# Kernel optimization log

Measured on AMD Instinct MI355X. Metric: run time of the kernel, lower is better.

## Reference

```python
import jax, jax.numpy as jnp
import numpy as np

B, T, E, H, V = 64, 32, 300, 1024, 10000


def setup_inputs() -> dict:
    key = jax.random.key(0)
    ks = jax.random.split(key, 12)
    s = lambda fan: 1.0 / np.sqrt(fan)
    return {
        "questions": jax.random.randint(ks[0], (B, T), 0, V, dtype=jnp.int64) if jax.config.jax_enable_x64 else jax.random.randint(ks[0], (B, T), 0, V, dtype=jnp.int32),
        "question_lengths": jax.random.randint(ks[1], (B,), 1, T + 1, dtype=jnp.int32),
        "embed_table": jax.random.normal(ks[2], (V, E), jnp.float32) * 0.02,
        "W_ih1": jax.random.normal(ks[3], (4 * H, E), jnp.float32) * s(H),
        "W_hh1": jax.random.normal(ks[4], (4 * H, H), jnp.float32) * s(H),
        "b_ih1": jax.random.normal(ks[5], (4 * H,), jnp.float32) * s(H),
        "b_hh1": jax.random.normal(ks[6], (4 * H,), jnp.float32) * s(H),
        "W_ih2": jax.random.normal(ks[7], (4 * H, H), jnp.float32) * s(H),
        "W_hh2": jax.random.normal(ks[8], (4 * H, H), jnp.float32) * s(H),
        "b_ih2": jax.random.normal(ks[9], (4 * H,), jnp.float32) * s(H),
        "b_hh2": jax.random.normal(ks[10], (4 * H,), jnp.float32) * s(H),
    }


def _lstm_cell(x_t, h, c, W_ih, W_hh, b_ih, b_hh):
    # PyTorch LSTMCell: gate order i, f, g, o
    gates = x_t @ W_ih.T + b_ih + h @ W_hh.T + b_hh  # [B, 4H]
    i, f, g, o = jnp.split(gates, 4, axis=-1)
    c_new = jax.nn.sigmoid(f) * c + jax.nn.sigmoid(i) * jnp.tanh(g)
    h_new = jax.nn.sigmoid(o) * jnp.tanh(c_new)
    return h_new, c_new


def reference(questions, question_lengths, embed_table,
              W_ih1, W_hh1, b_ih1, b_hh1, W_ih2, W_hh2, b_ih2, b_hh2):
    x = embed_table[questions]                      # [B, T, E]
    b, t, _ = x.shape
    h = W_hh1.shape[1]

    def step(carry, inp):
        h1, c1, h2, c2 = carry
        x_t, m = inp                                # x_t [B,E], m [B,1] bool
        h1n, c1n = _lstm_cell(x_t, h1, c1, W_ih1, W_hh1, b_ih1, b_hh1)
        h2n, c2n = _lstm_cell(h1n, h2, c2, W_ih2, W_hh2, b_ih2, b_hh2)
        # samples past their length keep their final state frozen
        h1 = jnp.where(m, h1n, h1); c1 = jnp.where(m, c1n, c1)
        h2 = jnp.where(m, h2n, h2); c2 = jnp.where(m, c2n, c2)
        return (h1, c1, h2, c2), None

    mask = jnp.arange(t)[None, :] < question_lengths[:, None]      # [B,T]
    xs = (jnp.swapaxes(x, 0, 1), jnp.swapaxes(mask, 0, 1)[..., None])
    init = tuple(jnp.zeros((b, h), x.dtype) for _ in range(4))
    (h1, c1, h2, c2), _ = jax.lax.scan(step, init, xs)

    # tile final top-layer hidden to [B, H, 28, 28]
    E_q = jnp.broadcast_to(h2[:, None, None, :], (b, 28, 28, h))
    E_q = jnp.transpose(E_q, (0, 3, 2, 1))
    return (E_q, h1[:, None, :], h2[:, None, :], c1[:, None, :], c2[:, None, :])
```

## Files before the change

### kernel.cpp

```cpp
#include <hip/hip_runtime.h>
#include <hip/hip_bf16.h>
#include <cstdint>

#define B_  64
#define T_  32
#define E_  300
#define EP  320
#define H_  1024
#define G4  4096
#define BH  65536
#define NBLK 192

typedef __attribute__((ext_vector_type(8))) short bf16x8;
typedef __attribute__((ext_vector_type(4))) float f32x4;
typedef unsigned short ushort_t;

__device__ __forceinline__ bf16x8 load_b8(const ushort_t* p) {
    union { uint4 u; bf16x8 v; } c;
    c.u = *reinterpret_cast<const uint4*>(p);
    return c.v;
}

__device__ __forceinline__ ushort_t f2bf(float x) {
    union { float f; uint32_t u; } c; c.f = x;
    uint32_t r = c.u + 0x7fffu + ((c.u >> 16) & 1u);
    return (ushort_t)(r >> 16);
}

__device__ __forceinline__ float sigm(float x) { return 1.0f / (1.0f + __expf(-x)); }

__device__ __forceinline__ void astore64(uint64_t* p, uint64_t v) {
    __hip_atomic_store(p, v, __ATOMIC_RELAXED, __HIP_MEMORY_SCOPE_AGENT);
}
__device__ __forceinline__ uint64_t packf2(float a, float b) {
    union { float f[2]; uint64_t u; } c; c.f[0] = a; c.f[1] = b; return c.u;
}

__device__ __forceinline__ void arrive(int* ctr, int t, int role, int js) {
    __hip_atomic_fetch_add(&ctr[((t * 3 + role) * 4 + (js & 3)) * 32], 1,
                           __ATOMIC_RELAXED, __HIP_MEMORY_SCOPE_AGENT);
}
__device__ __forceinline__ void waitc(int* ctr, int t, int role) {
    int sum;
    do {
        sum = 0;
        #pragma unroll
        for (int k = 0; k < 4; ++k)
            sum += __hip_atomic_load(&ctr[((t * 3 + role) * 4 + k) * 32],
                                     __ATOMIC_RELAXED, __HIP_MEMORY_SCOPE_AGENT);
        if (sum < 64) __builtin_amdgcn_s_sleep(1);
    } while (sum < 64);
}

__global__ void prep_inputs(const int* __restrict__ q, const float* __restrict__ table,
                            ushort_t* __restrict__ Xp,
                            const float* __restrict__ Wsrc, ushort_t* __restrict__ Wdst) {
    int blk = blockIdx.x;
    if (blk < 1280) {
        int i = blk * 256 + threadIdx.x;
        const int n = B_ * T_ * EP;
        for (; i < n; i += 1280 * 256) {
            int r = i / EP, c = i - r * EP;
            Xp[i] = (c < E_) ? f2bf(table[q[r] * E_ + c]) : (ushort_t)0;
        }
    } else {
        int i = (blk - 1280) * 256 + threadIdx.x;
        const int n = G4 * EP;
        for (; i < n; i += 2048 * 256) {
            int r = i / EP, c = i - r * EP;
            Wdst[i] = (c < E_) ? f2bf(Wsrc[r * E_ + c]) : (ushort_t)0;
        }
    }
}

__launch_bounds__(256)
__global__ void xgemm(const ushort_t* __restrict__ Xp, const ushort_t* __restrict__ Wp,
                      const float* __restrict__ b_ih1, const float* __restrict__ b_hh1,
                      float* __restrict__ xg) {
    int mblk = blockIdx.x, nblk = blockIdx.y;
    int wave = threadIdx.x >> 6, lane = threadIdx.x & 63;
    int lm = lane & 15, lq = lane >> 4;
    int m0 = mblk * 64 + wave * 16;
    f32x4 acc[4];
    #pragma unroll
    for (int g = 0; g < 4; ++g) {
        int n = nblk * 64 + g * 16 + lm;
        float bv = b_ih1[n] + b_hh1[n];
        acc[g] = (f32x4){bv, bv, bv, bv};
    }
    for (int k0 = 0; k0 < EP; k0 += 32) {
        bf16x8 a = load_b8(Xp + (m0 + lm) * EP + k0 + lq * 8);
        #pragma unroll
        for (int g = 0; g < 4; ++g) {
            bf16x8 b = load_b8(Wp + (nblk * 64 + g * 16 + lm) * EP + k0 + lq * 8);
            acc[g] = __builtin_amdgcn_mfma_f32_16x16x32_bf16(a, b, acc[g], 0, 0, 0);
        }
    }
    #pragma unroll
    for (int g = 0; g < 4; ++g)
        #pragma unroll
        for (int r = 0; r < 4; ++r) {
            int m = m0 + lq * 4 + r;
            int b = m >> 5, t = m & 31;
            int n = nblk * 64 + g * 16 + lm;
            xg[((size_t)t * B_ + b) * G4 + n] = acc[g][r];
        }
}


__device__ __forceinline__ void gemm_k1024(const ushort_t* __restrict__ hvec,
                                           const ushort_t (*w)[1032],
                                           int lm, int lq, int m0, f32x4 acc[4]) {
    const uint4* hr = reinterpret_cast<const uint4*>(hvec + (size_t)(m0 + lm) * H_);
    uint4 buf[32];
    #pragma unroll
    for (int grp = 0; grp < 4; ++grp)
        #pragma unroll
        for (int i = 0; i < 8; ++i)
            buf[grp * 8 + i] = hr[grp * 32 + i * 4 + lq];
    #pragma unroll
    for (int grp = 0; grp < 4; ++grp)
        #pragma unroll
        for (int i = 0; i < 8; ++i) {
            int k0 = grp * 256 + i * 32;
            union { uint4 u; bf16x8 v; } a; a.u = buf[grp * 8 + i];
            #pragma unroll
            for (int g = 0; g < 4; ++g) {
                bf16x8 bb = load_b8(&w[g * 16 + lm][k0 + lq * 8]);
                acc[g] = __builtin_amdgcn_mfma_f32_16x16x32_bf16(a.v, bb, acc[g], 0, 0, 0);
            }
        }
}

__device__ __forceinline__ void lstm_elem(const f32x4 acc[4], int r,
                                          float* c, float* h, ushort_t* hb) {
    float iv = sigm(acc[0][r]);
    float fv = sigm(acc[1][r]);
    float gv = tanhf(acc[2][r]);
    float ov = sigm(acc[3][r]);
    float cn = fv * c[r] + iv * gv;
    float hv = ov * tanhf(cn);
    c[r] = cn; h[r] = hv; hb[r] = f2bf(hv);
}

__device__ __forceinline__ void store_h_tile(ushort_t* dst, int js, const ushort_t* hst) {
    int tid = threadIdx.x;
    uint64_t v = reinterpret_cast<const uint64_t*>(hst)[tid];
    astore64(reinterpret_cast<uint64_t*>(dst + (size_t)(tid >> 2) * H_ + js * 16) + (tid & 3), v);
}

__global__ __launch_bounds__(256) void lstm_persist(
    const float* __restrict__ Whh1, const float* __restrict__ Wih2,
    const float* __restrict__ Whh2,
    const float* __restrict__ b_ih2, const float* __restrict__ b_hh2,
    const float* __restrict__ xg, const int* __restrict__ qlen,
    ushort_t* __restrict__ h1hist,
    ushort_t* __restrict__ h2hist,
    float* __restrict__ Qhist,
    float* __restrict__ h1f, float* __restrict__ c1f,
    float* __restrict__ h2f, float* __restrict__ c2f,
    int* __restrict__ ctr)
{
    __shared__ ushort_t ws[64][1032];
    __shared__ __align__(16) ushort_t hstage[64][16];

    const int blk  = blockIdx.x;
    const int role = blk >> 6;
    const int js   = blk & 63;
    const int wave = threadIdx.x >> 6, lane = threadIdx.x & 63;
    const int lm = lane & 15, lq = lane >> 4;
    const int m0 = wave * 16;

    const float* Wsrc = (role == 0) ? Whh1 : (role == 1) ? Wih2 : Whh2;
    for (int idx = threadIdx.x; idx < 64 * 256; idx += 256) {
        int r = idx >> 8, c4 = idx & 255;
        int grow = (r >> 4) * H_ + js * 16 + (r & 15);
        float4 v = reinterpret_cast<const float4*>(Wsrc + (size_t)grow * H_)[c4];
        uint2 pk;
        pk.x = (uint32_t)f2bf(v.x) | ((uint32_t)f2bf(v.y) << 16);
        pk.y = (uint32_t)f2bf(v.z) | ((uint32_t)f2bf(v.w) << 16);
        *reinterpret_cast<uint2*>(&ws[r][c4 * 4]) = pk;
    }
    __syncthreads();

    int q[4];
    #pragma unroll
    for (int r = 0; r < 4; ++r) q[r] = qlen[m0 + lq * 4 + r];

    float    c_reg[4]  = {0.f, 0.f, 0.f, 0.f};
    float    h_reg[4]  = {0.f, 0.f, 0.f, 0.f};
    ushort_t hb_reg[4] = {0, 0, 0, 0};

    if (role == 0) {
        for (int t = 0; t < T_; ++t) {
            f32x4 acc[4];
            #pragma unroll
            for (int g = 0; g < 4; ++g)
                #pragma unroll
                for (int r = 0; r < 4; ++r)
                    acc[g][r] = xg[((size_t)t * B_ + (m0 + lq * 4 + r)) * G4 + g * H_ + js * 16 + lm];
            if (t > 0) {
                if (threadIdx.x == 0) waitc(ctr, t - 1, 0);
                __syncthreads();
            }
            gemm_k1024(h1hist + (size_t)t * BH, ws, lm, lq, m0, acc);
            #pragma unroll
            for (int r = 0; r < 4; ++r) {
                if (t < q[r]) lstm_elem(acc, r, c_reg, h_reg, hb_reg);
                hstage[m0 + lq * 4 + r][lm] = hb_reg[r];
            }
            __syncthreads();
            store_h_tile(h1hist + (size_t)(t + 1) * BH, js, &hstage[0][0]);
            __syncthreads();
            if (threadIdx.x == 0) arrive(ctr, t, 0, js);
        }
        #pragma unroll
        for (int r = 0; r < 4; ++r) {
            int b = m0 + lq * 4 + r, j = js * 16 + lm;
            h1f[b * H_ + j] = h_reg[r]; c1f[b * H_ + j] = c_reg[r];
        }
    } else if (role == 1) {
        float bi[4];
        #pragma unroll
        for (int g = 0; g < 4; ++g) {
            int n = g * H_ + js * 16 + lm;
            bi[g] = b_ih2[n] + b_hh2[n];
        }
        for (int t = 0; t < T_; ++t) {
            if (threadIdx.x == 0) waitc(ctr, t, 0);
            __syncthreads();
            f32x4 acc[4];
            #pragma unroll
            for (int g = 0; g < 4; ++g) acc[g] = (f32x4){bi[g], bi[g], bi[g], bi[g]};
            gemm_k1024(h1hist + (size_t)(t + 1) * BH, ws, lm, lq, m0, acc);
            uint64_t* Qw64 = (uint64_t*)(Qhist + (size_t)t * (4 * BH));
            #pragma unroll
            for (int r = 0; r < 4; ++r) {
                int b = m0 + lq * 4 + r, j = js * 16 + lm;
                size_t base = ((size_t)b * H_ + j) * 2;
                astore64(Qw64 + base,     packf2(acc[0][r], acc[1][r]));
                astore64(Qw64 + base + 1, packf2(acc[2][r], acc[3][r]));
            }
            __syncthreads();
            if (threadIdx.x == 0) arrive(ctr, t, 1, js);
        }
    } else {
        for (int t = 0; t < T_; ++t) {
            if (threadIdx.x == 0) waitc(ctr, t, 1);
            else if (threadIdx.x == 64 && t > 0) waitc(ctr, t - 1, 2);
            __syncthreads();
            const uint4* Qr = (const uint4*)(Qhist + (size_t)t * (4 * BH));
            f32x4 acc[4];
            #pragma unroll
            for (int r = 0; r < 4; ++r) {
                uint4 p = Qr[(size_t)(m0 + lq * 4 + r) * H_ + js * 16 + lm];
                union { uint32_t u; float f; } x0, x1, x2, x3;
                x0.u = p.x; x1.u = p.y; x2.u = p.z; x3.u = p.w;
                acc[0][r] = x0.f; acc[1][r] = x1.f;
                acc[2][r] = x2.f; acc[3][r] = x3.f;
            }
            gemm_k1024(h2hist + (size_t)t * BH, ws, lm, lq, m0, acc);
            #pragma unroll
            for (int r = 0; r < 4; ++r) {
                if (t < q[r]) lstm_elem(acc, r, c_reg, h_reg, hb_reg);
                hstage[m0 + lq * 4 + r][lm] = hb_reg[r];
            }
            __syncthreads();
            store_h_tile(h2hist + (size_t)(t + 1) * BH, js, &hstage[0][0]);
            __syncthreads();
            if (t < T_ - 1 && threadIdx.x == 0) arrive(ctr, t, 2, js);
        }
        #pragma unroll
        for (int r = 0; r < 4; ++r) {
            int b = m0 + lq * 4 + r, j = js * 16 + lm;
            h2f[b * H_ + j] = h_reg[r]; c2f[b * H_ + j] = c_reg[r];
        }
    }
}

__global__ void write_out(const float* __restrict__ h1f, const float* __restrict__ h2f,
                          const float* __restrict__ c1f, const float* __restrict__ c2f,
                          float* __restrict__ out) {
    const long long EQ = (long long)B_ * H_ * 784;
    const long long n4 = (EQ + 4LL * B_ * H_) / 4;
    long long i4 = (long long)blockIdx.x * blockDim.x + threadIdx.x;
    long long stride = (long long)gridDim.x * blockDim.x;
    for (; i4 < n4; i4 += stride) {
        long long f = i4 * 4;
        float4 v;
        if (f < EQ) {
            long long bh = f / 784;
            float val = h2f[bh];
            v = make_float4(val, val, val, val);
        } else {
            long long r = f - EQ;
            int which = (int)(r >> 16);
            int j = (int)(r & 65535);
            const float* src = (which == 0) ? h1f : (which == 1) ? h2f : (which == 2) ? c1f : c2f;
            v = *reinterpret_cast<const float4*>(src + j);
        }
        reinterpret_cast<float4*>(out)[i4] = v;
    }
}

extern "C" void kernel_launch(void* const* d_in, const int* in_sizes, int n_in,
                              void* d_out, int out_size, void* d_ws, size_t ws_size,
                              hipStream_t stream) {
    const int*   questions = (const int*)d_in[0];
    const int*   qlen      = (const int*)d_in[1];
    const float* embed     = (const float*)d_in[2];
    const float* W_ih1     = (const float*)d_in[3];
    const float* W_hh1     = (const float*)d_in[4];
    const float* b_ih1     = (const float*)d_in[5];
    const float* b_hh1     = (const float*)d_in[6];
    const float* W_ih2     = (const float*)d_in[7];
    const float* W_hh2     = (const float*)d_in[8];
    const float* b_ih2     = (const float*)d_in[9];
    const float* b_hh2     = (const float*)d_in[10];
    float* out = (float*)d_out;

    char* w = (char*)d_ws;
    float*    xg     = (float*)(w + 0);
    ushort_t* Wih1p  = (ushort_t*)(w + 33554432);
    ushort_t* Xp     = (ushort_t*)(w + 36175872);
    int*      ctr    = (int*)(w + 36175872);
    ushort_t* h1hist = (ushort_t*)(w + 37486592);
    ushort_t* h2hist = (ushort_t*)(w + 41811968);
    float*    Qhist  = (float*)(w + 46137344);
    float*    h1f    = (float*)(w + 79691776);
    float*    c1f    = (float*)(w + 79953920);
    float*    h2f    = (float*)(w + 80216064);
    float*    c2f    = (float*)(w + 80478208);

    hipMemsetAsync(w + 37486592, 0, 131072, stream);
    hipMemsetAsync(w + 41811968, 0, 131072, stream);

    prep_inputs<<<3328, 256, 0, stream>>>(questions, embed, Xp, W_ih1, Wih1p);
    xgemm<<<dim3(32, 64), 256, 0, stream>>>(Xp, Wih1p, b_ih1, b_hh1, xg);

    hipMemsetAsync(w + 36175872, 0, 49152, stream);

    lstm_persist<<<NBLK, 256, 0, stream>>>(W_hh1, W_ih2, W_hh2, b_ih2, b_hh2,
                                           xg, qlen,
                                           h1hist, h2hist, Qhist,
                                           h1f, c1f, h2f, c2f, ctr);

    write_out<<<4096, 256, 0, stream>>>(h1f, h2f, c1f, c2f, out);
}
```

Baseline: 635.7 us.

## Replace atomic counter barriers with per-block step flags polled by a wave

Swaps the per-step atomic fetch-add counters, which one thread polled, for per-block monotonic step flags. A whole wave polls all 64 producer flags in parallel and checks them with a wave-wide vote. The layer-2 block now issues its Q-history load before the recurrent GEMM and adds it afterwards, so the load latency overlaps the matrix work. The flag wait also gains a bounded spin guard that silently proceeds on timeout, which could hide a deadlock as wrong results.

```diff
diff --git a/kernel.cpp b/kernel.cpp
--- a/kernel.cpp
+++ b/kernel.cpp
@@ -36,20 +36,19 @@
     union { float f[2]; uint64_t u; } c; c.f[0] = a; c.f[1] = b; return c.u;
 }
 
-__device__ __forceinline__ void arrive(int* ctr, int t, int role, int js) {
-    __hip_atomic_fetch_add(&ctr[((t * 3 + role) * 4 + (js & 3)) * 32], 1,
-                           __ATOMIC_RELAXED, __HIP_MEMORY_SCOPE_AGENT);
-}
-__device__ __forceinline__ void waitc(int* ctr, int t, int role) {
-    int sum;
-    do {
-        sum = 0;
-        #pragma unroll
-        for (int k = 0; k < 4; ++k)
-            sum += __hip_atomic_load(&ctr[((t * 3 + role) * 4 + k) * 32],
-                                     __ATOMIC_RELAXED, __HIP_MEMORY_SCOPE_AGENT);
-        if (sum < 64) __builtin_amdgcn_s_sleep(1);
-    } while (sum < 64);
+__device__ __forceinline__ void setflag(int* flags, int role, int js, int val) {
+    __hip_atomic_store(&flags[(role * 64 + js) * 16], val,
+                       __ATOMIC_RELAXED, __HIP_MEMORY_SCOPE_AGENT);
+}
+__device__ __forceinline__ void waitwave(const int* flags, int role, int target, int lane) {
+    const int* p = &flags[(role * 64 + lane) * 16];
+    int guard = 0;
+    for (;;) {
+        int v = __hip_atomic_load(p, __ATOMIC_RELAXED, __HIP_MEMORY_SCOPE_AGENT);
+        if (__all(v >= target)) return;
+        if (++guard > (1 << 22)) return;
+        __builtin_amdgcn_s_sleep(1);
+    }
 }
 
 __global__ void prep_inputs(const int* __restrict__ q, const float* __restrict__ table,
@@ -159,7 +158,7 @@
     float* __restrict__ Qhist,
     float* __restrict__ h1f, float* __restrict__ c1f,
     float* __restrict__ h2f, float* __restrict__ c2f,
-    int* __restrict__ ctr)
+    int* __restrict__ flags)
 {
     __shared__ ushort_t ws[64][1032];
     __shared__ __align__(16) ushort_t hstage[64][16];
@@ -200,7 +199,7 @@
                 for (int r = 0; r < 4; ++r)
                     acc[g][r] = xg[((size_t)t * B_ + (m0 + lq * 4 + r)) * G4 + g * H_ + js * 16 + lm];
             if (t > 0) {
-                if (threadIdx.x == 0) waitc(ctr, t - 1, 0);
+                if (wave == 0) waitwave(flags, 0, t, lane);
                 __syncthreads();
             }
             gemm_k1024(h1hist + (size_t)t * BH, ws, lm, lq, m0, acc);
@@ -212,7 +211,7 @@
             __syncthreads();
             store_h_tile(h1hist + (size_t)(t + 1) * BH, js, &hstage[0][0]);
             __syncthreads();
-            if (threadIdx.x == 0) arrive(ctr, t, 0, js);
+            if (threadIdx.x == 0) setflag(flags, 0, js, t + 1);
         }
         #pragma unroll
         for (int r = 0; r < 4; ++r) {
@@ -227,7 +226,7 @@
             bi[g] = b_ih2[n] + b_hh2[n];
         }
         for (int t = 0; t < T_; ++t) {
-            if (threadIdx.x == 0) waitc(ctr, t, 0);
+            if (wave == 0) waitwave(flags, 0, t + 1, lane);
             __syncthreads();
             f32x4 acc[4];
             #pragma unroll
@@ -242,24 +241,33 @@
                 astore64(Qw64 + base + 1, packf2(acc[2][r], acc[3][r]));
             }
             __syncthreads();
-            if (threadIdx.x == 0) arrive(ctr, t, 1, js);
+            if (threadIdx.x == 0) setflag(flags, 1, js, t + 1);
         }
     } else {
         for (int t = 0; t < T_; ++t) {
-            if (threadIdx.x == 0) waitc(ctr, t, 1);
-            else if (threadIdx.x == 64 && t > 0) waitc(ctr, t - 1, 2);
+            if (t > 0) {
+                if (wave == 0)      waitwave(flags, 1, t + 1, lane);
+                else if (wave == 1) waitwave(flags, 2, t,     lane);
+            } else {
+                if (wave == 0)      waitwave(flags, 1, 1,     lane);
+            }
             __syncthreads();
             const uint4* Qr = (const uint4*)(Qhist + (size_t)t * (4 * BH));
+            uint4 qp[4];
+            #pragma unroll
+            for (int r = 0; r < 4; ++r)
+                qp[r] = Qr[(size_t)(m0 + lq * 4 + r) * H_ + js * 16 + lm];
             f32x4 acc[4];
             #pragma unroll
+            for (int g = 0; g < 4; ++g) acc[g] = (f32x4){0.f, 0.f, 0.f, 0.f};
+            gemm_k1024(h2hist + (size_t)t * BH, ws, lm, lq, m0, acc);
+            #pragma unroll
             for (int r = 0; r < 4; ++r) {
-                uint4 p = Qr[(size_t)(m0 + lq * 4 + r) * H_ + js * 16 + lm];
                 union { uint32_t u; float f; } x0, x1, x2, x3;
-                x0.u = p.x; x1.u = p.y; x2.u = p.z; x3.u = p.w;
-                acc[0][r] = x0.f; acc[1][r] = x1.f;
-                acc[2][r] = x2.f; acc[3][r] = x3.f;
-            }
-            gemm_k1024(h2hist + (size_t)t * BH, ws, lm, lq, m0, acc);
+                x0.u = qp[r].x; x1.u = qp[r].y; x2.u = qp[r].z; x3.u = qp[r].w;
+                acc[0][r] += x0.f; acc[1][r] += x1.f;
+                acc[2][r] += x2.f; acc[3][r] += x3.f;
+            }
             #pragma unroll
             for (int r = 0; r < 4; ++r) {
                 if (t < q[r]) lstm_elem(acc, r, c_reg, h_reg, hb_reg);
@@ -268,7 +276,7 @@
             __syncthreads();
             store_h_tile(h2hist + (size_t)(t + 1) * BH, js, &hstage[0][0]);
             __syncthreads();
-            if (t < T_ - 1 && threadIdx.x == 0) arrive(ctr, t, 2, js);
+            if (t < T_ - 1 && threadIdx.x == 0) setflag(flags, 2, js, t + 1);
         }
         #pragma unroll
         for (int r = 0; r < 4; ++r) {
@@ -323,7 +331,7 @@
     float*    xg     = (float*)(w + 0);
     ushort_t* Wih1p  = (ushort_t*)(w + 33554432);
     ushort_t* Xp     = (ushort_t*)(w + 36175872);
-    int*      ctr    = (int*)(w + 36175872);
+    int*      flags  = (int*)(w + 36175872);
     ushort_t* h1hist = (ushort_t*)(w + 37486592);
     ushort_t* h2hist = (ushort_t*)(w + 41811968);
     float*    Qhist  = (float*)(w + 46137344);
@@ -338,12 +346,12 @@
     prep_inputs<<<3328, 256, 0, stream>>>(questions, embed, Xp, W_ih1, Wih1p);
     xgemm<<<dim3(32, 64), 256, 0, stream>>>(Xp, Wih1p, b_ih1, b_hh1, xg);
 
-    hipMemsetAsync(w + 36175872, 0, 49152, stream);
+    hipMemsetAsync(w + 36175872, 0, 12288, stream);
 
     lstm_persist<<<NBLK, 256, 0, stream>>>(W_hh1, W_ih2, W_hh2, b_ih2, b_hh2,
                                            xg, qlen,
                                            h1hist, h2hist, Qhist,
-                                           h1f, c1f, h2f, c2f, ctr);
+                                           h1f, c1f, h2f, c2f, flags);
 
     write_out<<<4096, 256, 0, stream>>>(h1f, h2f, c1f, c2f, out);
 }
```

After: 631.9 us. About the same (-0.6%).
